# Kernel tuning notes

Measured on AMD Instinct MI355X. Metric: run time of the kernel, lower is better.

## Reference

```python
import jax, jax.numpy as jnp
import numpy as np

NV, NA, T, FD, C, E = 192, 64, 128, 1024, 128, 262144
SPK = 3
N = (NV + NA) * T  # 32768 total graph nodes
NEG = -1e30


def _seg_max(msg, dst, mask):
    # masked scatter-max; PyG fills segments with no messages with 0
    m = jnp.where(mask[:, None], msg, NEG)
    out = jax.ops.segment_max(m, dst, num_segments=N)
    return jnp.where(out > NEG * 0.5, out, 0.0)


def _edge_conv(x, src, dst, mask, W1, b1, W2, b2):
    # EdgeConv: max_j MLP(cat[x_i, x_j - x_i])
    xi = x[dst]
    h = jnp.concatenate([xi, x[src] - xi], axis=-1)  # [E, 2C]
    h = jax.nn.relu(h @ W1 + b1) @ W2 + b2
    return _seg_max(h, dst, mask)


def _sage_conv(x, src, dst, mask, Wl, bl, Wr):
    # SAGEConv: lin_l(mean_j x_j) + lin_r(x_i), lin_r has no bias
    mf = mask.astype(x.dtype)
    s = jax.ops.segment_sum(x[src] * mf[:, None], dst, num_segments=N)
    cnt = jax.ops.segment_sum(mf, dst, num_segments=N)
    mean = s / jnp.maximum(cnt, 1.0)[:, None]
    return mean @ Wl + bl + x @ Wr


def setup_inputs():
    ks = jax.random.split(jax.random.key(0), 24)
    s = 0.05
    vals = jnp.array([-3, -2, -1, 0, 1, 3], jnp.int32)
    return {
        "x_visual": jax.random.normal(ks[0], (NV, T, FD), jnp.float32),
        "x_audio": jax.random.normal(ks[1], (NA, T, FD), jnp.float32),
        "W011": jax.random.normal(ks[2], (FD, C)) * s, "b011": jnp.zeros((C,)),
        "W012": jax.random.normal(ks[3], (FD, C)) * s, "b012": jnp.zeros((C,)),
        "ecA_W1": jax.random.normal(ks[4], (2 * C, C)) * s, "ecA_b1": jnp.zeros((C,)),
        "ecA_W2": jax.random.normal(ks[5], (C, C)) * s, "ecA_b2": jnp.zeros((C,)),
        "ec1_W1": jax.random.normal(ks[6], (2 * C, C)) * s, "ec1_b1": jnp.zeros((C,)),
        "ec1_W2": jax.random.normal(ks[7], (C, C)) * s, "ec1_b2": jnp.zeros((C,)),
        "ec2_W1": jax.random.normal(ks[8], (2 * C, C)) * s, "ec2_b1": jnp.zeros((C,)),
        "ec2_W2": jax.random.normal(ks[9], (C, C)) * s, "ec2_b2": jnp.zeros((C,)),
        "ec3_W1": jax.random.normal(ks[10], (2 * C, C)) * s, "ec3_b1": jnp.zeros((C,)),
        "ec3_W2": jax.random.normal(ks[11], (C, C)) * s, "ec3_b2": jnp.zeros((C,)),
        "sage_Wl": jax.random.normal(ks[12], (C, C)) * s, "sage_bl": jnp.zeros((C,)),
        "sage_Wr": jax.random.normal(ks[13], (C, C)) * s,
        "fc_W": jax.random.normal(ks[14], (C, 1)) * s, "fc_b": jnp.zeros((1,)),
        "edge_index": jax.random.randint(ks[15], (2, E), 0, N, dtype=jnp.int32),
        "edge_attr": vals[jax.random.randint(ks[16], (E,), 0, 6)],
        "speakers": SPK,
    }


def reference(x_visual, x_audio, W011, b011, W012, b012,
              ecA_W1, ecA_b1, ecA_W2, ecA_b2,
              ec1_W1, ec1_b1, ec1_W2, ec1_b2,
              ec2_W1, ec2_b1, ec2_W2, ec2_b2,
              ec3_W1, ec3_b1, ec3_W2, ec3_b2,
              sage_Wl, sage_bl, sage_Wr, fc_W, fc_b,
              edge_index, edge_attr, speakers):
    xv = x_visual @ W011 + b011          # [NV, T, C]
    xa = x_audio @ W012 + b012           # [NA, T, C]
    x = jnp.concatenate([xv, xa], axis=0).reshape(-1, C)  # [N, C]
    src, dst = edge_index[0], edge_index[1]
    m_audio = edge_attr == -2
    m_vpa = edge_attr == -3
    m_acv = edge_attr == 3
    m1 = (edge_attr >= 0) & (edge_attr <= 1)
    m2 = (edge_attr <= 0) & (edge_attr >= -1)
    m3 = jnp.abs(edge_attr) <= 1
    # Visual_Add_Audio_GNN: max-aggregate (x_i + x_j)
    xa_g = jax.nn.relu(_seg_max(x[dst] + x[src], dst, m_vpa))
    a = jax.nn.relu(_edge_conv(xa_g, src, dst, m_audio, ecA_W1, ecA_b1, ecA_W2, ecA_b2))
    a_res = a @ fc_W + fc_b              # [N, 1] per-node audio scores
    # Audio_Weight_Add_Visual_GNN: sum-aggregate (w_j * x_j + x_i)
    wmsg = jnp.where(m_acv[:, None], a_res[src] * x[src] + x[dst], 0.0)
    xv2 = jax.nn.relu(jax.ops.segment_sum(wmsg, dst, num_segments=N))

    def branch(mask, W1, b1, W2, b2):
        h = jax.nn.relu(_edge_conv(xv2, src, dst, mask, W1, b1, W2, b2))
        return jax.nn.relu(_sage_conv(h, src, dst, mask, sage_Wl, sage_bl, sage_Wr))

    xo = (branch(m1, ec1_W1, ec1_b1, ec1_W2, ec1_b2)
          + branch(m2, ec2_W1, ec2_b1, ec2_W2, ec2_b2)
          + branch(m3, ec3_W1, ec3_b1, ec3_W2, ec3_b2))
    # gather main-speaker visual nodes
    idx = (jnp.arange(0, NV * T, speakers * T)[:, None] + jnp.arange(T)).reshape(-1)
    return xo[idx]
```

## Files before the change

### kernel.cpp

```cpp
#include <hip/hip_runtime.h>
#include <cstdint>
#include <cstddef>

#define NVv 192
#define NAa 64
#define TT 128
#define FDd 1024
#define CCc 128
#define EEe 262144
#define NNn 32768

typedef _Float16 f16x8 __attribute__((ext_vector_type(8)));
typedef float f32x4 __attribute__((ext_vector_type(4)));

#define CAP0 65536
#define CAP1 65536
#define CAP2 65536
#define CAP3 98304
#define CAP4 98304
#define CAP5 147456
#define ARENA_TOTAL (CAP0+CAP1+CAP2+CAP3+CAP4+CAP5)

__device__ __forceinline__ void eval_masks(int a, bool m[6]) {
    m[0] = (a == -3); m[1] = (a == -2); m[2] = (a == 3);
    m[3] = (a >= 0) & (a <= 1);
    m[4] = (a >= -1) & (a <= 0);
    m[5] = (a >= -1) & (a <= 1);
}

__global__ __launch_bounds__(256) void k_zero(float* __restrict__ p) {
    size_t i = (size_t)blockIdx.x * 1024 + (size_t)threadIdx.x * 4;
    *(float4*)(p + i) = make_float4(0.f, 0.f, 0.f, 0.f);
}

__global__ __launch_bounds__(256) void k_wprep_big(
    const float* __restrict__ W011, const float* __restrict__ W012,
    _Float16* __restrict__ dst)
{
    int idx = blockIdx.x * 256 + threadIdx.x;
    int which = idx >> 17;
    int r = idx & 131071;
    int n = r >> 10, k = r & 1023;
    const float* src = which ? W012 : W011;
    dst[idx] = (_Float16)src[k * 128 + n];
}

struct WSmall { const float* p[14]; };

__global__ __launch_bounds__(256) void k_wprep_small(WSmall ws, _Float16* __restrict__ dst)
{
    int idx = blockIdx.x * 256 + threadIdx.x;
    int seg = idx >> 14;
    int r = idx & 16383;
    int n = r >> 7, k = r & 127;
    const float* src = ws.p[seg];
    float v = src[k * 128 + n];
    if (seg < 12 && (seg % 3) == 0) v -= src[16384 + k * 128 + n];
    dst[idx] = (_Float16)v;
}

__global__ __launch_bounds__(256) void k_hist(
    const int* __restrict__ attr, const int* __restrict__ edst,
    int* __restrict__ hist)
{
    int e = blockIdx.x * 256 + threadIdx.x;
    int a = attr[e], d = edst[e];
    bool m[6]; eval_masks(a, m);
#pragma unroll
    for (int j = 0; j < 6; ++j)
        if (m[j]) atomicAdd(&hist[j * NNn + d], 1);
}

__global__ __launch_bounds__(256) void k_scan_a(
    const int* __restrict__ hist, int* __restrict__ base, int* __restrict__ bsum)
{
    __shared__ int wsum[4];
    int bid = blockIdx.x;
    int idx = bid * 256 + threadIdx.x;
    int tid = threadIdx.x, lane = tid & 63, wv = tid >> 6;
    int v = hist[idx];
    int x = v;
#pragma unroll
    for (int off = 1; off < 64; off <<= 1) {
        int y = __shfl_up(x, off, 64);
        if (lane >= off) x += y;
    }
    if (lane == 63) wsum[wv] = x;
    __syncthreads();
    int add = 0;
    for (int w = 0; w < wv; ++w) add += wsum[w];
    base[idx] = add + x - v;
    if (tid == 255) bsum[bid] = add + x;
}

__global__ __launch_bounds__(384) void k_scan_b(int* __restrict__ bsum, int* __restrict__ cnts)
{
    int wv = threadIdx.x >> 6;
    int lane = threadIdx.x & 63;
    int run = 0;
#pragma unroll
    for (int c0 = 0; c0 < 128; c0 += 64) {
        int v = bsum[wv * 128 + c0 + lane];
        int x = v;
#pragma unroll
        for (int off = 1; off < 64; off <<= 1) {
            int y = __shfl_up(x, off, 64);
            if (lane >= off) x += y;
        }
        bsum[wv * 128 + c0 + lane] = run + (x - v);
        run += __shfl(x, 63, 64);
    }
    if (lane == 0) cnts[wv] = run;
}

__global__ __launch_bounds__(256) void k_scan_c(int* __restrict__ base, const int* __restrict__ bsum)
{
    base[blockIdx.x * 256 + threadIdx.x] += bsum[blockIdx.x];
}

__global__ __launch_bounds__(256) void k_fill(
    const int* __restrict__ esrc, const int* __restrict__ edst,
    const int* __restrict__ attr, const int* __restrict__ base,
    int* __restrict__ fill, int2* __restrict__ arena)
{
    int e = blockIdx.x * 256 + threadIdx.x;
    int a = attr[e];
    int s = esrc[e], d = edst[e];
    bool m[6]; eval_masks(a, m);
    const int caps[6] = {CAP0, CAP1, CAP2, CAP3, CAP4, CAP5};
    const int offs[6] = {0, CAP0, CAP0+CAP1, CAP0+CAP1+CAP2,
                         CAP0+CAP1+CAP2+CAP3, CAP0+CAP1+CAP2+CAP3+CAP4};
#pragma unroll
    for (int j = 0; j < 6; ++j) {
        if (m[j]) {
            int pos = base[j * NNn + d] + atomicAdd(&fill[j * NNn + d], 1);
            if (pos < caps[j]) arena[offs[j] + pos] = make_int2(s, d);
        }
    }
}

__global__ __launch_bounds__(256) void k_gemm(
    const float* __restrict__ A, const _Float16* __restrict__ BT,
    const float* __restrict__ bias, void* __restrict__ out,
    const _Float16* __restrict__ BT2, void* __restrict__ out2,
    int M, int K, int do_relu, int f16out)
{
    __shared__ _Float16 Al[64][40];
    __shared__ _Float16 Bl[128][40];
    __shared__ _Float16 Bl2[128][40];
    const int tid  = threadIdx.x;
    const int wave = tid >> 6;
    const int lane = tid & 63;
    const int m0   = blockIdx.x * 64;

    f32x4 acc[8], acc2[8];
#pragma unroll
    for (int i = 0; i < 8; ++i) { acc[i] = (f32x4){0,0,0,0}; acc2[i] = (f32x4){0,0,0,0}; }

    const int ar = tid >> 2;
    const int ak = (tid & 3) * 8;
    const int fr = wave * 16 + (lane & 15);
    const int fk = (lane >> 4) * 8;

    for (int k0 = 0; k0 < K; k0 += 32) {
        const float* asrc = A + (size_t)(m0 + ar) * K + (k0 + ak);
        float4 a0 = *(const float4*)asrc;
        float4 a1 = *(const float4*)(asrc + 4);
        f16x8 av = { (_Float16)a0.x, (_Float16)a0.y, (_Float16)a0.z, (_Float16)a0.w,
                     (_Float16)a1.x, (_Float16)a1.y, (_Float16)a1.z, (_Float16)a1.w };
        *(f16x8*)&Al[ar][ak] = av;
#pragma unroll
        for (int i = 0; i < 2; ++i) {
            int c = tid + i * 256;
            int n = c >> 2, koff = (c & 3) * 8;
            *(f16x8*)&Bl[n][koff] = *(const f16x8*)(BT + (size_t)n * K + k0 + koff);
            if (out2)
                *(f16x8*)&Bl2[n][koff] = *(const f16x8*)(BT2 + (size_t)n * K + k0 + koff);
        }
        __syncthreads();
        f16x8 af = *(const f16x8*)&Al[fr][fk];
#pragma unroll
        for (int nt = 0; nt < 8; ++nt) {
            f16x8 bf = *(const f16x8*)&Bl[nt * 16 + (lane & 15)][fk];
            acc[nt] = __builtin_amdgcn_mfma_f32_16x16x32_f16(af, bf, acc[nt], 0, 0, 0);
        }
        if (out2) {
#pragma unroll
            for (int nt = 0; nt < 8; ++nt) {
                f16x8 bf = *(const f16x8*)&Bl2[nt * 16 + (lane & 15)][fk];
                acc2[nt] = __builtin_amdgcn_mfma_f32_16x16x32_f16(af, bf, acc2[nt], 0, 0, 0);
            }
        }
        __syncthreads();
    }

    const int rbase = wave * 16 + (lane >> 4) * 4;
    const int cbase = lane & 15;
#pragma unroll
    for (int nt = 0; nt < 8; ++nt) {
        int col = nt * 16 + cbase;
        float bv = bias ? bias[col] : 0.f;
#pragma unroll
        for (int rr = 0; rr < 4; ++rr) {
            int gr = m0 + rbase + rr;
            size_t o = (size_t)gr * 128 + col;
            float v = acc[nt][rr] + bv;
            if (do_relu) v = fmaxf(v, 0.f);
            if (f16out) {
                ((_Float16*)out)[o] = (_Float16)v;
                if (out2) ((_Float16*)out2)[o] = (_Float16)acc2[nt][rr];
            } else {
                ((float*)out)[o] = v;
                if (out2) ((float*)out2)[o] = acc2[nt][rr];
            }
        }
    }
}

__global__ __launch_bounds__(256, 3) void k_edge_mlp(
    const _Float16* __restrict__ P, const _Float16* __restrict__ V,
    const _Float16* __restrict__ W2T, const float* __restrict__ b2,
    const int2* __restrict__ list, const int* __restrict__ cntp, int cap,
    float* __restrict__ agg)
{
    __shared__ _Float16 Rl[64][136];
    __shared__ _Float16 W2l[128][136];
    __shared__ float b2l[128];
    __shared__ int2 eSD[64];
    __shared__ unsigned char gstart[66];
    __shared__ int gdst[64];
    __shared__ int ngrS;

    int cnt = min(*cntp, cap);
    int ntiles = (cnt + 63) >> 6;
    if ((int)blockIdx.x >= ntiles) return;

    const int tid  = threadIdx.x;
    const int wave = tid >> 6;
    const int lane = tid & 63;

#pragma unroll
    for (int i = 0; i < 8; ++i) {
        int c = tid + i * 256;
        int n = c >> 4, koff = (c & 15) * 8;
        *(f16x8*)&W2l[n][koff] = *(const f16x8*)(W2T + n * 128 + koff);
    }
    if (tid < 128) b2l[tid] = b2[tid];

    const int col   = tid & 127;
    const int half  = tid >> 7;
    const int frow  = wave * 16 + (lane & 15);
    const int fq    = (lane >> 4) * 8;
    const int rbase = wave * 16 + (lane >> 4) * 4;
    const int cbase = lane & 15;
    const int rrow  = tid >> 4;
    const int rch   = (tid & 15) * 8;

    for (int t = blockIdx.x; t < ntiles; t += gridDim.x) {
        __syncthreads();
        if (tid < 64) {
            int e = t * 64 + tid;
            eSD[tid] = (e < cnt) ? list[e] : make_int2(0, -1);
        }
        __syncthreads();
        if (tid < 64) {
            int d = eSD[tid].y;
            bool flag = (tid == 0) || (d != eSD[tid - 1].y);
            unsigned long long bm = __ballot(flag);
            int rank = (int)__popcll(bm & ((1ull << tid) - 1ull));
            if (flag) { gstart[rank] = (unsigned char)tid; gdst[rank] = d; }
            if (tid == 0) {
                int ng = (int)__popcll(bm);
                ngrS = ng;
                gstart[ng] = 64;
            }
        }
#pragma unroll
        for (int p = 0; p < 4; ++p) {
            int i = p * 16 + rrow;
            int2 sd = eSD[i];
            f16x8 rv = {0, 0, 0, 0, 0, 0, 0, 0};
            if (sd.y >= 0) {
                f16x8 pv = *(const f16x8*)(P + (size_t)sd.y * 128 + rch);
                f16x8 vv = *(const f16x8*)(V + (size_t)sd.x * 128 + rch);
                rv = pv + vv;
#pragma unroll
                for (int q = 0; q < 8; ++q)
                    rv[q] = (rv[q] > (_Float16)0.f) ? rv[q] : (_Float16)0.f;
            }
            *(f16x8*)&Rl[i][rch] = rv;
        }
        __syncthreads();

        f32x4 acc[8];
#pragma unroll
        for (int i = 0; i < 8; ++i) acc[i] = (f32x4){0,0,0,0};
#pragma unroll
        for (int t4 = 0; t4 < 4; ++t4) {
            f16x8 af = *(const f16x8*)&Rl[frow][t4 * 32 + fq];
#pragma unroll
            for (int nt = 0; nt < 8; ++nt) {
                f16x8 bf = *(const f16x8*)&W2l[nt * 16 + (lane & 15)][t4 * 32 + fq];
                acc[nt] = __builtin_amdgcn_mfma_f32_16x16x32_f16(af, bf, acc[nt], 0, 0, 0);
            }
        }
        __syncthreads();
#pragma unroll
        for (int nt = 0; nt < 8; ++nt) {
            int c2 = nt * 16 + cbase;
            float bv = b2l[c2];
#pragma unroll
            for (int rr = 0; rr < 4; ++rr)
                Rl[rbase + rr][c2] = (_Float16)fmaxf(acc[nt][rr] + bv, 0.f);
        }
        __syncthreads();
        int ng = ngrS;
        for (int g = half; g < ng; g += 2) {
            int s = gstart[g], e = gstart[g + 1];
            int d = gdst[g];
            if (d < 0) continue;
            float m = 0.f;
            for (int i = s; i < e; ++i)
                m = fmaxf(m, (float)Rl[i][col]);
            size_t o = (size_t)d * 128 + col;
            if (s == 0 || e == 64)
                atomicMax((unsigned int*)&agg[o], __float_as_uint(m));
            else
                agg[o] = m;
        }
    }
}

__global__ __launch_bounds__(256) void k_csr_vpa(
    const float* __restrict__ X, const int2* __restrict__ list,
    const int* __restrict__ base, const int* __restrict__ cntarr, int cap,
    float* __restrict__ S)
{
    int col = threadIdx.x & 127;
    int sub = threadIdx.x >> 7;
    for (int d = blockIdx.x * 2 + sub; d < NNn; d += gridDim.x * 2) {
        int c = cntarr[d];
        float v = 0.f;
        if (c > 0) {
            int b = base[d];
            int end = min(b + c, cap);
            float mx = -3.0e38f;
            for (int i = b; i < end; ++i)
                mx = fmaxf(mx, X[(size_t)list[i].x * 128 + col]);
            v = fmaxf(X[(size_t)d * 128 + col] + mx, 0.f);
        }
        S[(size_t)d * 128 + col] = v;
    }
}

__global__ __launch_bounds__(256) void k_csr_acv(
    const float* __restrict__ X, const float* __restrict__ ares,
    const int2* __restrict__ list,
    const int* __restrict__ base, const int* __restrict__ cntarr, int cap,
    float* __restrict__ S)
{
    int col = threadIdx.x & 127;
    int sub = threadIdx.x >> 7;
    for (int d = blockIdx.x * 2 + sub; d < NNn; d += gridDim.x * 2) {
        int c = cntarr[d];
        float v = 0.f;
        if (c > 0) {
            int b = base[d];
            int end = min(b + c, cap);
            float s = 0.f;
            for (int i = b; i < end; ++i) {
                int sr = list[i].x;
                s += ares[sr] * X[(size_t)sr * 128 + col];
            }
            v = fmaxf(s + (float)c * X[(size_t)d * 128 + col], 0.f);
        }
        S[(size_t)d * 128 + col] = v;
    }
}

__global__ __launch_bounds__(256) void k_csr_meanc(
    const float* __restrict__ AH, const int2* __restrict__ list,
    const int* __restrict__ basej, const int* __restrict__ histj, int cap,
    const int* __restrict__ spk, int ntarg,
    float* __restrict__ S1c, float* __restrict__ AHc)
{
    int col = threadIdx.x & 127;
    int sub = threadIdx.x >> 7;
    int step = spk[0] * TT;
    for (int ci = blockIdx.x * 2 + sub; ci < ntarg; ci += gridDim.x * 2) {
        int d = (ci >> 7) * step + (ci & 127);
        int c = histj[d];
        float v = 0.f;
        if (c > 0) {
            int b = basej[d];
            int end = min(b + c, cap);
            float s = 0.f;
            for (int i = b; i < end; ++i)
                s += AH[(size_t)list[i].x * 128 + col];
            v = s / (float)c;
        }
        S1c[(size_t)ci * 128 + col] = v;
        AHc[(size_t)ci * 128 + col] = AH[(size_t)d * 128 + col];
    }
}

__global__ __launch_bounds__(256) void k_fc(
    const float* __restrict__ A, const float* __restrict__ W,
    const float* __restrict__ b, float* __restrict__ ares)
{
    int node = blockIdx.x * 4 + (threadIdx.x >> 6);
    int lane = threadIdx.x & 63;
    const float* row = A + (size_t)node * 128;
    float v = row[lane] * W[lane] + row[lane + 64] * W[lane + 64];
#pragma unroll
    for (int off = 32; off > 0; off >>= 1) v += __shfl_down(v, off, 64);
    if (lane == 0) ares[node] = v + b[0];
}

__global__ __launch_bounds__(256) void k_sage_out(
    const float* __restrict__ S1c, const float* __restrict__ AHc,
    const _Float16* __restrict__ WlT, const _Float16* __restrict__ WrT,
    const float* __restrict__ bl, float* __restrict__ out, int ntarg)
{
    __shared__ _Float16 Al[64][40];
    __shared__ _Float16 Bl[128][40];
    const int tid  = threadIdx.x;
    const int wave = tid >> 6;
    const int lane = tid & 63;
    const int m0   = blockIdx.x * 64;

    f32x4 accB[8], accO[8];
#pragma unroll
    for (int i = 0; i < 8; ++i) { accB[i] = (f32x4){0,0,0,0}; accO[i] = (f32x4){0,0,0,0}; }

    const int ar = tid >> 2;
    const int ak = (tid & 3) * 8;
    const int fr = wave * 16 + (lane & 15);
    const int fk = (lane >> 4) * 8;
    const int rbase = wave * 16 + (lane >> 4) * 4;
    const int cbase = lane & 15;

    for (int seg = 0; seg < 6; ++seg) {
        int b = seg >> 1, which = seg & 1;
        const float* A = (which ? AHc : S1c) + (size_t)b * ntarg * 128;
        const _Float16* BT = which ? WrT : WlT;
        for (int k0 = 0; k0 < 128; k0 += 32) {
            __syncthreads();
            const float* asrc = A + (size_t)(m0 + ar) * 128 + (k0 + ak);
            float4 a0 = *(const float4*)asrc;
            float4 a1 = *(const float4*)(asrc + 4);
            f16x8 av = { (_Float16)a0.x, (_Float16)a0.y, (_Float16)a0.z, (_Float16)a0.w,
                         (_Float16)a1.x, (_Float16)a1.y, (_Float16)a1.z, (_Float16)a1.w };
            *(f16x8*)&Al[ar][ak] = av;
#pragma unroll
            for (int i = 0; i < 2; ++i) {
                int c = tid + i * 256;
                int n = c >> 2, koff = (c & 3) * 8;
                *(f16x8*)&Bl[n][koff] = *(const f16x8*)(BT + (size_t)n * 128 + k0 + koff);
            }
            __syncthreads();
            f16x8 af = *(const f16x8*)&Al[fr][fk];
#pragma unroll
            for (int nt = 0; nt < 8; ++nt) {
                f16x8 bf = *(const f16x8*)&Bl[nt * 16 + (lane & 15)][fk];
                accB[nt] = __builtin_amdgcn_mfma_f32_16x16x32_f16(af, bf, accB[nt], 0, 0, 0);
            }
        }
        if (which) {
#pragma unroll
            for (int nt = 0; nt < 8; ++nt) {
                int col = nt * 16 + cbase;
                float bv = bl[col];
#pragma unroll
                for (int rr = 0; rr < 4; ++rr) {
                    accO[nt][rr] += fmaxf(accB[nt][rr] + bv, 0.f);
                    accB[nt][rr] = 0.f;
                }
            }
        }
    }
#pragma unroll
    for (int nt = 0; nt < 8; ++nt) {
        int col = nt * 16 + cbase;
#pragma unroll
        for (int rr = 0; rr < 4; ++rr)
            out[(size_t)(m0 + rbase + rr) * 128 + col] = accO[nt][rr];
    }
}

extern "C" void kernel_launch(void* const* d_in, const int* in_sizes, int n_in,
                              void* d_out, int out_size, void* d_ws, size_t ws_size,
                              hipStream_t stream)
{
    (void)in_sizes; (void)n_in; (void)ws_size;
    const float* xv   = (const float*)d_in[0];
    const float* xa   = (const float*)d_in[1];
    const float* W011 = (const float*)d_in[2];
    const float* b011 = (const float*)d_in[3];
    const float* W012 = (const float*)d_in[4];
    const float* b012 = (const float*)d_in[5];
    const float* ecW1[4] = {(const float*)d_in[6],  (const float*)d_in[10],
                            (const float*)d_in[14], (const float*)d_in[18]};
    const float* ecb1[4] = {(const float*)d_in[7],  (const float*)d_in[11],
                            (const float*)d_in[15], (const float*)d_in[19]};
    const float* ecW2[4] = {(const float*)d_in[8],  (const float*)d_in[12],
                            (const float*)d_in[16], (const float*)d_in[20]};
    const float* ecb2[4] = {(const float*)d_in[9],  (const float*)d_in[13],
                            (const float*)d_in[17], (const float*)d_in[21]};
    const float* sageWl = (const float*)d_in[22];
    const float* sagebl = (const float*)d_in[23];
    const float* sageWr = (const float*)d_in[24];
    const float* fcW    = (const float*)d_in[25];
    const float* fcb    = (const float*)d_in[26];
    const int*   esrc   = (const int*)d_in[27];
    const int*   edst   = esrc + EEe;
    const int*   attr   = (const int*)d_in[28];
    const int*   spk    = (const int*)d_in[29];
    float* out = (float*)d_out;
    const int ntarg = out_size >> 7;

    const size_t NC = (size_t)NNn * CCc;
    float* ws   = (float*)d_ws;
    float* X    = ws;
    float* S1   = ws + 1 * NC;
    float* AH   = ws + 2 * NC;
    float* XV2  = ws + 3 * NC;
    float* AHc  = ws + 4 * NC;
    _Float16* P16 = (_Float16*)(ws + 5 * NC);
    _Float16* V16 = P16 + NC;
    float* ARES = ws + 6 * NC;
    int*   cnts = (int*)(ARES + NNn);
    int*   bsum = cnts + 16;
    int*   hist = bsum + 1024;
    int*   fill = hist + 6 * NNn;
    int*   base = fill + 6 * NNn;
    int2*  arena = (int2*)(base + 6 * NNn);
    _Float16* WT = (_Float16*)(arena + ARENA_TOTAL);

    const int offs[6] = {0, CAP0, CAP0+CAP1, CAP0+CAP1+CAP2,
                         CAP0+CAP1+CAP2+CAP3, CAP0+CAP1+CAP2+CAP3+CAP4};
    const int caps[6] = {CAP0, CAP1, CAP2, CAP3, CAP4, CAP5};

    const _Float16* W011T = WT;
    const _Float16* W012T = WT + 131072;
    const _Float16* WTs   = WT + 262144;
    const _Float16* WlT   = WTs + 12 * 16384;
    const _Float16* WrT   = WTs + 13 * 16384;

    const int GN  = NNn / 64;
    const int GNC = (int)(NC / 1024);

    k_wprep_big<<<1024, 256, 0, stream>>>(W011, W012, WT);
    WSmall wsm;
    for (int i = 0; i < 4; ++i) {
        wsm.p[3*i + 0] = ecW1[i];
        wsm.p[3*i + 1] = ecW1[i] + 16384;
        wsm.p[3*i + 2] = ecW2[i];
    }
    wsm.p[12] = sageWl; wsm.p[13] = sageWr;
    k_wprep_small<<<896, 256, 0, stream>>>(wsm, (_Float16*)WTs);
    k_zero<<<(2 * 6 * NNn) / 1024, 256, 0, stream>>>((float*)hist);
    k_hist<<<EEe / 256, 256, 0, stream>>>(attr, edst, hist);
    k_scan_a<<<768, 256, 0, stream>>>(hist, base, bsum);
    k_scan_b<<<1, 384, 0, stream>>>(bsum, cnts);
    k_scan_c<<<768, 256, 0, stream>>>(base, bsum);
    k_fill<<<EEe / 256, 256, 0, stream>>>(esrc, edst, attr, base, fill, arena);

    k_gemm<<<NVv * TT / 64, 256, 0, stream>>>(xv, W011T, b011, X,
                                              nullptr, nullptr, NVv * TT, FDd, 0, 0);
    k_gemm<<<NAa * TT / 64, 256, 0, stream>>>(xa, W012T, b012,
                                              X + (size_t)NVv * TT * CCc,
                                              nullptr, nullptr, NAa * TT, FDd, 0, 0);
    k_csr_vpa<<<2048, 256, 0, stream>>>(X, arena + offs[0], base + 0 * NNn,
                                        hist + 0 * NNn, caps[0], S1);
    k_gemm<<<GN, 256, 0, stream>>>(S1, WTs, ecb1[0], P16,
                                   WTs + 16384, V16, NNn, CCc, 0, 1);
    k_zero<<<GNC, 256, 0, stream>>>(AH);
    k_edge_mlp<<<2048, 256, 0, stream>>>(P16, V16, WTs + 2 * 16384, ecb2[0],
                                         arena + offs[1], cnts + 1, caps[1], AH);
    k_fc<<<NNn / 4, 256, 0, stream>>>(AH, fcW, fcb, ARES);
    k_csr_acv<<<2048, 256, 0, stream>>>(X, ARES, arena + offs[2], base + 2 * NNn,
                                        hist + 2 * NNn, caps[2], XV2);
    for (int b = 0; b < 3; ++b) {
        int j = 3 + b;
        const _Float16* Wd = WTs + (3 * (b + 1)) * 16384;
        k_gemm<<<GN, 256, 0, stream>>>(XV2, Wd, ecb1[b + 1], P16,
                                       Wd + 16384, V16, NNn, CCc, 0, 1);
        k_zero<<<GNC, 256, 0, stream>>>(AH);
        k_edge_mlp<<<2048, 256, 0, stream>>>(P16, V16, Wd + 2 * 16384, ecb2[b + 1],
                                             arena + offs[j], cnts + j, caps[j], AH);
        k_csr_meanc<<<2048, 256, 0, stream>>>(AH, arena + offs[j], base + j * NNn,
                                              hist + j * NNn, caps[j], spk, ntarg,
                                              S1 + (size_t)b * ntarg * 128,
                                              AHc + (size_t)b * ntarg * 128);
    }
    k_sage_out<<<ntarg / 64, 256, 0, stream>>>(S1, AHc, WlT, WrT, sagebl, out, ntarg);
}
```

Before: 600.8 us.

## Replace generic GEMM with specialized projection and P/V kernels, zero only needed rows

The generic k_gemm is replaced by two specialized kernels. k_proj merges the visual and audio 1024-wide projections into one launch, using 128-row tiles and 128-wide K chunks held in LDS. k_pv computes the two 128x128 products with both weight matrices resident in LDS, registers holding A, and writes go through LDS staging to vectorized stores. The full zeroing of the aggregation buffer is replaced by k_zero_need, which zeroes only nodes with no edges or whose edge range crosses a 64-edge tile boundary. This relies on the edge-MLP kernel fully overwriting the rows it owns exclusively, which is an implicit correctness coupling.

```diff
diff --git a/kernel.cpp b/kernel.cpp
--- a/kernel.cpp
+++ b/kernel.cpp
@@ -31,6 +31,23 @@
 __global__ __launch_bounds__(256) void k_zero(float* __restrict__ p) {
     size_t i = (size_t)blockIdx.x * 1024 + (size_t)threadIdx.x * 4;
     *(float4*)(p + i) = make_float4(0.f, 0.f, 0.f, 0.f);
+}
+
+__global__ __launch_bounds__(256) void k_zero_need(
+    const int* __restrict__ histj, const int* __restrict__ basej,
+    float* __restrict__ AH)
+{
+    int col = threadIdx.x & 127, sub = threadIdx.x >> 7;
+    for (int d = blockIdx.x * 2 + sub; d < NNn; d += gridDim.x * 2) {
+        int c = histj[d];
+        bool need;
+        if (c == 0) need = true;
+        else {
+            int b = basej[d], e = b + c;
+            need = ((b & 63) == 0) || ((e & 63) == 0) || ((b >> 6) != ((e - 1) >> 6));
+        }
+        if (need) AH[(size_t)d * 128 + col] = 0.f;
+    }
 }
 
 __global__ __launch_bounds__(256) void k_wprep_big(
@@ -139,81 +156,146 @@
     }
 }
 
-__global__ __launch_bounds__(256) void k_gemm(
-    const float* __restrict__ A, const _Float16* __restrict__ BT,
-    const float* __restrict__ bias, void* __restrict__ out,
-    const _Float16* __restrict__ BT2, void* __restrict__ out2,
-    int M, int K, int do_relu, int f16out)
-{
-    __shared__ _Float16 Al[64][40];
-    __shared__ _Float16 Bl[128][40];
-    __shared__ _Float16 Bl2[128][40];
-    const int tid  = threadIdx.x;
-    const int wave = tid >> 6;
-    const int lane = tid & 63;
-    const int m0   = blockIdx.x * 64;
-
-    f32x4 acc[8], acc2[8];
-#pragma unroll
-    for (int i = 0; i < 8; ++i) { acc[i] = (f32x4){0,0,0,0}; acc2[i] = (f32x4){0,0,0,0}; }
-
-    const int ar = tid >> 2;
-    const int ak = (tid & 3) * 8;
-    const int fr = wave * 16 + (lane & 15);
+__global__ __launch_bounds__(512) void k_proj(
+    const float* __restrict__ xv, const float* __restrict__ xa,
+    const _Float16* __restrict__ BTv, const _Float16* __restrict__ BTa,
+    const float* __restrict__ bv_, const float* __restrict__ ba_,
+    float* __restrict__ X)
+{
+    __shared__ _Float16 Bl[128][136];
+    __shared__ float Hs[8][16][132];
+    __shared__ float bb[128];
+    const int tid = threadIdx.x, wave = tid >> 6, lane = tid & 63;
+    const int blk = blockIdx.x;
+    const float* A; const _Float16* BT; const float* bias; int mbase, obase;
+    if (blk < 192) { A = xv; BT = BTv; bias = bv_; mbase = blk * 128; obase = mbase; }
+    else { A = xa; BT = BTa; bias = ba_; mbase = (blk - 192) * 128; obase = 24576 + mbase; }
+    if (tid < 128) bb[tid] = bias[tid];
+
+    const int mrow = mbase + wave * 16 + (lane & 15);
+    const int fk   = (lane >> 4) * 8;
+    f32x4 acc[8];
+#pragma unroll
+    for (int i = 0; i < 8; ++i) acc[i] = (f32x4){0,0,0,0};
+
+    for (int kc = 0; kc < 8; ++kc) {
+        __syncthreads();
+#pragma unroll
+        for (int it = 0; it < 4; ++it) {
+            int c = it * 512 + tid;
+            int n = c >> 4, koff = (c & 15) * 8;
+            *(f16x8*)&Bl[n][koff] = *(const f16x8*)(BT + (size_t)n * 1024 + kc * 128 + koff);
+        }
+        __syncthreads();
+        f16x8 af[4];
+#pragma unroll
+        for (int t4 = 0; t4 < 4; ++t4) {
+            const float* asrc = A + (size_t)mrow * 1024 + kc * 128 + t4 * 32 + fk;
+            float4 a0 = *(const float4*)asrc;
+            float4 a1 = *(const float4*)(asrc + 4);
+            af[t4] = (f16x8){ (_Float16)a0.x, (_Float16)a0.y, (_Float16)a0.z, (_Float16)a0.w,
+                              (_Float16)a1.x, (_Float16)a1.y, (_Float16)a1.z, (_Float16)a1.w };
+        }
+#pragma unroll
+        for (int t4 = 0; t4 < 4; ++t4)
+#pragma unroll
+            for (int nt = 0; nt < 8; ++nt) {
+                f16x8 bf = *(const f16x8*)&Bl[nt * 16 + (lane & 15)][t4 * 32 + fk];
+                acc[nt] = __builtin_amdgcn_mfma_f32_16x16x32_f16(af[t4], bf, acc[nt], 0, 0, 0);
+            }
+    }
+    const int cbase = lane & 15, rloc = (lane >> 4) * 4;
+#pragma unroll
+    for (int nt = 0; nt < 8; ++nt) {
+        int c2 = nt * 16 + cbase;
+        float bvv = bb[c2];
+#pragma unroll
+        for (int rr = 0; rr < 4; ++rr)
+            Hs[wave][rloc + rr][c2] = acc[nt][rr] + bvv;
+    }
+#pragma unroll
+    for (int it = 0; it < 8; ++it) {
+        int id = it * 64 + lane;
+        int row = id >> 5, off = (id & 31) * 4;
+        float4 v = *(float4*)&Hs[wave][row][off];
+        *(float4*)&X[(size_t)(obase + wave * 16 + row) * 128 + off] = v;
+    }
+}
+
+__global__ __launch_bounds__(512) void k_pv(
+    const float* __restrict__ A,
+    const _Float16* __restrict__ BT1, const float* __restrict__ b1,
+    const _Float16* __restrict__ BT2,
+    _Float16* __restrict__ P, _Float16* __restrict__ V)
+{
+    __shared__ _Float16 Bl1[128][136];
+    __shared__ _Float16 Bl2[128][136];
+    __shared__ _Float16 Hs[8][16][136];
+    __shared__ float bb[128];
+    const int tid = threadIdx.x, wave = tid >> 6, lane = tid & 63;
+    const int r0 = blockIdx.x * 128 + wave * 16;
+
+#pragma unroll
+    for (int it = 0; it < 4; ++it) {
+        int c = it * 512 + tid;
+        int n = c >> 4, koff = (c & 15) * 8;
+        *(f16x8*)&Bl1[n][koff] = *(const f16x8*)(BT1 + (size_t)n * 128 + koff);
+        *(f16x8*)&Bl2[n][koff] = *(const f16x8*)(BT2 + (size_t)n * 128 + koff);
+    }
+    if (tid < 128) bb[tid] = b1[tid];
+    __syncthreads();
+
     const int fk = (lane >> 4) * 8;
-
-    for (int k0 = 0; k0 < K; k0 += 32) {
-        const float* asrc = A + (size_t)(m0 + ar) * K + (k0 + ak);
+    const int mrow = r0 + (lane & 15);
+    f16x8 af[4];
+#pragma unroll
+    for (int t4 = 0; t4 < 4; ++t4) {
+        const float* asrc = A + (size_t)mrow * 128 + t4 * 32 + fk;
         float4 a0 = *(const float4*)asrc;
         float4 a1 = *(const float4*)(asrc + 4);
-        f16x8 av = { (_Float16)a0.x, (_Float16)a0.y, (_Float16)a0.z, (_Float16)a0.w,
-                     (_Float16)a1.x, (_Float16)a1.y, (_Float16)a1.z, (_Float16)a1.w };
-        *(f16x8*)&Al[ar][ak] = av;
-#pragma unroll
-        for (int i = 0; i < 2; ++i) {
-            int c = tid + i * 256;
-            int n = c >> 2, koff = (c & 3) * 8;
-            *(f16x8*)&Bl[n][koff] = *(const f16x8*)(BT + (size_t)n * K + k0 + koff);
-            if (out2)
-                *(f16x8*)&Bl2[n][koff] = *(const f16x8*)(BT2 + (size_t)n * K + k0 + koff);
-        }
-        __syncthreads();
-        f16x8 af = *(const f16x8*)&Al[fr][fk];
+        af[t4] = (f16x8){ (_Float16)a0.x, (_Float16)a0.y, (_Float16)a0.z, (_Float16)a0.w,
+                          (_Float16)a1.x, (_Float16)a1.y, (_Float16)a1.z, (_Float16)a1.w };
+    }
+    f32x4 acc1[8], acc2[8];
+#pragma unroll
+    for (int i = 0; i < 8; ++i) { acc1[i] = (f32x4){0,0,0,0}; acc2[i] = (f32x4){0,0,0,0}; }
+#pragma unroll
+    for (int t4 = 0; t4 < 4; ++t4)
 #pragma unroll
         for (int nt = 0; nt < 8; ++nt) {
-            f16x8 bf = *(const f16x8*)&Bl[nt * 16 + (lane & 15)][fk];
-            acc[nt] = __builtin_amdgcn_mfma_f32_16x16x32_f16(af, bf, acc[nt], 0, 0, 0);
-        }
-        if (out2) {
-#pragma unroll
-            for (int nt = 0; nt < 8; ++nt) {
-                f16x8 bf = *(const f16x8*)&Bl2[nt * 16 + (lane & 15)][fk];
-                acc2[nt] = __builtin_amdgcn_mfma_f32_16x16x32_f16(af, bf, acc2[nt], 0, 0, 0);
-            }
-        }
-        __syncthreads();
-    }
-
-    const int rbase = wave * 16 + (lane >> 4) * 4;
-    const int cbase = lane & 15;
+            f16x8 bf1 = *(const f16x8*)&Bl1[nt * 16 + (lane & 15)][t4 * 32 + fk];
+            f16x8 bf2 = *(const f16x8*)&Bl2[nt * 16 + (lane & 15)][t4 * 32 + fk];
+            acc1[nt] = __builtin_amdgcn_mfma_f32_16x16x32_f16(af[t4], bf1, acc1[nt], 0, 0, 0);
+            acc2[nt] = __builtin_amdgcn_mfma_f32_16x16x32_f16(af[t4], bf2, acc2[nt], 0, 0, 0);
+        }
+
+    const int cbase = lane & 15, rloc = (lane >> 4) * 4;
 #pragma unroll
     for (int nt = 0; nt < 8; ++nt) {
-        int col = nt * 16 + cbase;
-        float bv = bias ? bias[col] : 0.f;
-#pragma unroll
-        for (int rr = 0; rr < 4; ++rr) {
-            int gr = m0 + rbase + rr;
-            size_t o = (size_t)gr * 128 + col;
-            float v = acc[nt][rr] + bv;
-            if (do_relu) v = fmaxf(v, 0.f);
-            if (f16out) {
-                ((_Float16*)out)[o] = (_Float16)v;
-                if (out2) ((_Float16*)out2)[o] = (_Float16)acc2[nt][rr];
-            } else {
-                ((float*)out)[o] = v;
-                if (out2) ((float*)out2)[o] = acc2[nt][rr];
-            }
-        }
+        int c2 = nt * 16 + cbase;
+        float bvv = bb[c2];
+#pragma unroll
+        for (int rr = 0; rr < 4; ++rr)
+            Hs[wave][rloc + rr][c2] = (_Float16)(acc1[nt][rr] + bvv);
+    }
+#pragma unroll
+    for (int it = 0; it < 4; ++it) {
+        int id = it * 64 + lane;
+        int row = id >> 4, koff = (id & 15) * 8;
+        *(f16x8*)&P[(size_t)(r0 + row) * 128 + koff] = *(f16x8*)&Hs[wave][row][koff];
+    }
+#pragma unroll
+    for (int nt = 0; nt < 8; ++nt) {
+        int c2 = nt * 16 + cbase;
+#pragma unroll
+        for (int rr = 0; rr < 4; ++rr)
+            Hs[wave][rloc + rr][c2] = (_Float16)acc2[nt][rr];
+    }
+#pragma unroll
+    for (int it = 0; it < 4; ++it) {
+        int id = it * 64 + lane;
+        int row = id >> 4, koff = (id & 15) * 8;
+        *(f16x8*)&V[(size_t)(r0 + row) * 128 + koff] = *(f16x8*)&Hs[wave][row][koff];
     }
 }
 
@@ -547,9 +629,6 @@
     const _Float16* WlT   = WTs + 12 * 16384;
     const _Float16* WrT   = WTs + 13 * 16384;
 
-    const int GN  = NNn / 64;
-    const int GNC = (int)(NC / 1024);
-
     k_wprep_big<<<1024, 256, 0, stream>>>(W011, W012, WT);
     WSmall wsm;
     for (int i = 0; i < 4; ++i) {
@@ -566,16 +645,11 @@
     k_scan_c<<<768, 256, 0, stream>>>(base, bsum);
     k_fill<<<EEe / 256, 256, 0, stream>>>(esrc, edst, attr, base, fill, arena);
 
-    k_gemm<<<NVv * TT / 64, 256, 0, stream>>>(xv, W011T, b011, X,
-                                              nullptr, nullptr, NVv * TT, FDd, 0, 0);
-    k_gemm<<<NAa * TT / 64, 256, 0, stream>>>(xa, W012T, b012,
-                                              X + (size_t)NVv * TT * CCc,
-                                              nullptr, nullptr, NAa * TT, FDd, 0, 0);
+    k_proj<<<256, 512, 0, stream>>>(xv, xa, W011T, W012T, b011, b012, X);
     k_csr_vpa<<<2048, 256, 0, stream>>>(X, arena + offs[0], base + 0 * NNn,
                                         hist + 0 * NNn, caps[0], S1);
-    k_gemm<<<GN, 256, 0, stream>>>(S1, WTs, ecb1[0], P16,
-                                   WTs + 16384, V16, NNn, CCc, 0, 1);
-    k_zero<<<GNC, 256, 0, stream>>>(AH);
+    k_pv<<<256, 512, 0, stream>>>(S1, WTs, ecb1[0], WTs + 16384, P16, V16);
+    k_zero_need<<<2048, 256, 0, stream>>>(hist + 1 * NNn, base + 1 * NNn, AH);
     k_edge_mlp<<<2048, 256, 0, stream>>>(P16, V16, WTs + 2 * 16384, ecb2[0],
                                          arena + offs[1], cnts + 1, caps[1], AH);
     k_fc<<<NNn / 4, 256, 0, stream>>>(AH, fcW, fcb, ARES);
@@ -584,9 +658,8 @@
     for (int b = 0; b < 3; ++b) {
         int j = 3 + b;
         const _Float16* Wd = WTs + (3 * (b + 1)) * 16384;
-        k_gemm<<<GN, 256, 0, stream>>>(XV2, Wd, ecb1[b + 1], P16,
-                                       Wd + 16384, V16, NNn, CCc, 0, 1);
-        k_zero<<<GNC, 256, 0, stream>>>(AH);
+        k_pv<<<256, 512, 0, stream>>>(XV2, Wd, ecb1[b + 1], Wd + 16384, P16, V16);
+        k_zero_need<<<2048, 256, 0, stream>>>(hist + j * NNn, base + j * NNn, AH);
         k_edge_mlp<<<2048, 256, 0, stream>>>(P16, V16, Wd + 2 * 16384, ecb2[b + 1],
                                              arena + offs[j], cnts + j, caps[j], AH);
         k_csr_meanc<<<2048, 256, 0, stream>>>(AH, arena + offs[j], base + j * NNn,
```

Result: faster. 550.3 us (-8.4%).
